# Kernel optimization log

Hardware: AMD Instinct MI355X
Metric: run time of the kernel (lower is better)

The kernel has to match this reference:

```python
import jax, jax.numpy as jnp
import numpy as np


def _ln(x, g, b, eps=1e-5):
    m = x.mean(-1, keepdims=True)
    v = ((x - m) ** 2).mean(-1, keepdims=True)
    return g * (x - m) / jnp.sqrt(v + eps) + b


def _mha(x, w_qkv, b_qkv, w_o, b_o, nh):
    B, S, d = x.shape
    hd = d // nh
    qkv = x @ w_qkv.T + b_qkv
    q, k, v = jnp.split(qkv, 3, axis=-1)
    sp = lambda t: t.reshape(B, S, nh, hd).transpose(0, 2, 1, 3)
    q, k, v = sp(q), sp(k), sp(v)
    a = jax.nn.softmax(jnp.einsum('bhqd,bhkd->bhqk', q, k) / np.float32(np.sqrt(hd)), axis=-1)
    o = jnp.einsum('bhqk,bhkd->bhqd', a, v).transpose(0, 2, 1, 3).reshape(B, S, d)
    return o @ w_o.T + b_o


def _enc(x, w_qkv, b_qkv, w_o, b_o, ga, ba, wf1, bf1, wf2, bf2, gb, bb, nh=2):
    # torch TransformerEncoderLayer, post-norm, ReLU FFN
    x = _ln(x + _mha(x, w_qkv, b_qkv, w_o, b_o, nh), ga, ba)
    ff = jax.nn.relu(x @ wf1.T + bf1) @ wf2.T + bf2
    return _ln(x + ff, gb, bb)


def forward(nodes, w_qkv1, b_qkv1, w_o1, b_o1, g1a, bb1a, w_ff1a, bf1a, w_ff1b, bf1b, g1b, bb1b,
            wq, bq, wk, bk, wv, bv, g_co, bb_co, w4, b4, w5, b5, w6, b6,
            w_rel, w_root, b_rgcn, wg_rel, wg_root, bg,
            w_qkv2, b_qkv2, w_o2, b_o2, g2a, bb2a, w_ff2a, bf2a, w_ff2b, bf2b, g2b, bb2b,
            w_l1, b_l1, w_l2, b_l2, edge_index, opt_idx):
    N, H = nodes.shape
    O = 4
    B = opt_idx.shape[0] // O
    # option-node mutual attention (encoder_layer1) + scatter back
    opts = nodes[opt_idx].reshape(B, O, H)
    opts = _enc(opts, w_qkv1, b_qkv1, w_o1, b_o1, g1a, bb1a, w_ff1a, bf1a, w_ff1b, bf1b, g1b, bb1b)
    nodes2 = nodes.at[opt_idx].set(opts.reshape(B * O, H))
    src, dst = edge_index[0], edge_index[1]
    xs, xd = nodes2[src], nodes2[dst]  # [E,H]
    # per-edge 4-head co-attention: node1/node2 are single rows so qk^T is a scalar per head
    hd = H // 4
    q = (xs @ wq.T + bq).reshape(-1, 4, hd)
    k = (xd @ wk.T + bk).reshape(-1, 4, hd)
    v = (xd @ wv.T + bv).reshape(-1, 4, hd)
    s = jnp.einsum('ehd,ehd->eh', q, k) / np.float32(np.sqrt(hd))
    r = (s[..., None] * v).reshape(-1, H)
    co = jax.nn.relu(_ln(r, g_co, bb_co))
    h = jax.nn.relu(co @ w4.T + b4)
    h = jax.nn.relu(h @ w5.T + b5)
    logits = h @ w6.T + b6  # [E,8]
    # original applies Softmax(dim=0) to a [1,8] tensor -> all ones -> argmax picks class 0
    probs = jax.nn.softmax(logits[:, None, :], axis=1)[:, 0, :]
    edge_type = jnp.argmax(probs, axis=-1)
    # RGCNConv(H, H, num_relations=8), mean aggregation per relation + root + bias
    agg = jnp.zeros((N, H), nodes.dtype)
    for rel in range(8):
        m = edge_type == rel
        msg = jnp.where(m[:, None], xs @ w_rel[rel], 0.0)
        ssum = jax.ops.segment_sum(msg, dst, num_segments=N)
        cnt = jax.ops.segment_sum(m.astype(nodes.dtype), dst, num_segments=N)
        agg = agg + ssum / jnp.maximum(cnt, 1.0)[:, None]
    out1 = nodes2 @ w_root + b_rgcn + agg
    # GraphConv(H, 64): add-aggregated neighbors through lin_rel + root through lin_root
    agg2 = jax.ops.segment_sum(out1[src], dst, num_segments=N)
    out2 = agg2 @ wg_rel + bg + out1 @ wg_root  # [N,64]
    # readout over option nodes (encoder_layer2 + tanh(linear1) + linear2)
    opt2 = out2[opt_idx].reshape(B, O, 64)
    opt2 = _enc(opt2, w_qkv2, b_qkv2, w_o2, b_o2, g2a, bb2a, w_ff2a, bf2a, w_ff2b, bf2b, g2b, bb2b)
    opt2 = jnp.tanh(opt2 @ w_l1.T + b_l1)
    return opt2 @ w_l2.T + b_l2  # [B,O,1]


def setup_inputs() -> dict:
    key = jax.random.key(0)
    N, E, B, O, H, F = 20000, 40000, 64, 4, 768, 2048
    ks = iter(jax.random.split(key, 64))
    W = lambda *s: jax.random.normal(next(ks), s, jnp.float32) * 0.02
    return dict(
        nodes=jax.random.normal(next(ks), (N, H), jnp.float32),
        edge_index=jax.random.randint(next(ks), (2, E), 0, N),
        opt_idx=jnp.arange(B * O),
        w_qkv1=W(3 * H, H), b_qkv1=jnp.zeros(3 * H), w_o1=W(H, H), b_o1=jnp.zeros(H),
        g1a=jnp.ones(H), bb1a=jnp.zeros(H),
        w_ff1a=W(F, H), bf1a=jnp.zeros(F), w_ff1b=W(H, F), bf1b=jnp.zeros(H),
        g1b=jnp.ones(H), bb1b=jnp.zeros(H),
        wq=W(H, H), bq=jnp.zeros(H), wk=W(H, H), bk=jnp.zeros(H), wv=W(H, H), bv=jnp.zeros(H),
        g_co=jnp.ones(H), bb_co=jnp.zeros(H),
        w4=W(H, H), b4=jnp.zeros(H), w5=W(64, H), b5=jnp.zeros(64), w6=W(8, 64), b6=jnp.zeros(8),
        w_rel=W(8, H, H), w_root=W(H, H), b_rgcn=jnp.zeros(H),
        wg_rel=W(H, 64), wg_root=W(H, 64), bg=jnp.zeros(64),
        w_qkv2=W(192, 64), b_qkv2=jnp.zeros(192), w_o2=W(64, 64), b_o2=jnp.zeros(64),
        g2a=jnp.ones(64), bb2a=jnp.zeros(64),
        w_ff2a=W(F, 64), bf2a=jnp.zeros(F), w_ff2b=W(64, F), bf2b=jnp.zeros(64),
        g2b=jnp.ones(64), bb2b=jnp.zeros(64),
        w_l1=W(64, 64), b_l1=jnp.zeros(64), w_l2=W(1, 64), b_l2=jnp.zeros(1),
    )


def reference(nodes, edge_index, opt_idx, w_qkv1, b_qkv1, w_o1, b_o1, g1a, bb1a, w_ff1a, bf1a,
              w_ff1b, bf1b, g1b, bb1b, wq, bq, wk, bk, wv, bv, g_co, bb_co, w4, b4, w5, b5, w6, b6,
              w_rel, w_root, b_rgcn, wg_rel, wg_root, bg, w_qkv2, b_qkv2, w_o2, b_o2, g2a, bb2a,
              w_ff2a, bf2a, w_ff2b, bf2b, g2b, bb2b, w_l1, b_l1, w_l2, b_l2):
    return forward(nodes, w_qkv1, b_qkv1, w_o1, b_o1, g1a, bb1a, w_ff1a, bf1a, w_ff1b, bf1b, g1b,
                   bb1b, wq, bq, wk, bk, wv, bv, g_co, bb_co, w4, b4, w5, b5, w6, b6, w_rel, w_root,
                   b_rgcn, wg_rel, wg_root, bg, w_qkv2, b_qkv2, w_o2, b_o2, g2a, bb2a, w_ff2a, bf2a,
                   w_ff2b, bf2b, g2b, bb2b, w_l1, b_l1, w_l2, b_l2, edge_index, opt_idx)
```

## Files before the change

### kernel.cpp

```cpp
#include <hip/hip_runtime.h>

typedef unsigned short u16;
typedef unsigned int u32;
typedef __bf16 bf16x8 __attribute__((ext_vector_type(8)));
typedef float f32x4 __attribute__((ext_vector_type(4)));

__device__ __forceinline__ u16 f2bf(float f) {
    union { float f; u32 u; } v; v.f = f;
    u32 r = v.u + 0x7FFFu + ((v.u >> 16) & 1u);
    return (u16)(r >> 16);
}
__device__ __forceinline__ float bf2f(u16 h) {
    union { u32 u; float f; } v; v.u = (u32)h << 16; return v.f;
}

__global__ __launch_bounds__(256) void gemm_bt(
    const u16* __restrict__ A, const u16* __restrict__ Bt,
    float* __restrict__ C, u16* __restrict__ Cb, const float* __restrict__ bias,
    int M, int N, int K, int relu)
{
    __shared__ char lA[128 * 64 * 2];
    __shared__ char lB[128 * 64 * 2];
    const int t = threadIdx.x;
    const int w = t >> 6, l = t & 63;
    const int bn = blockIdx.x, bm = blockIdx.y;
    const int wr = w >> 1, wc = w & 1;

    const int srow = w * 8 + (l >> 3);
    const int scol = ((l & 7) ^ (l >> 3)) << 3;
    const u16* gA = A + (size_t)(bm * 128 + srow) * K + scol;
    const u16* gB = Bt + (size_t)(bn * 128 + srow) * K + scol;

    f32x4 zero = {0.f, 0.f, 0.f, 0.f};
    f32x4 acc[4][4];
#pragma unroll
    for (int i = 0; i < 4; i++)
#pragma unroll
        for (int j = 0; j < 4; j++) acc[i][j] = zero;

    const int arow = wr * 64 + (l & 15);
    const int brow = wc * 64 + (l & 15);
    const int kx = l >> 4;
    const int sw = l & 7;

    for (int k0 = 0; k0 < K; k0 += 64) {
#pragma unroll
        for (int c2 = 0; c2 < 4; ++c2) {
            __builtin_amdgcn_global_load_lds(
                (const __attribute__((address_space(1))) void*)(gA + (size_t)c2 * 32 * K + k0),
                (__attribute__((address_space(3))) void*)(lA + c2 * 4096 + w * 1024), 16, 0, 0);
            __builtin_amdgcn_global_load_lds(
                (const __attribute__((address_space(1))) void*)(gB + (size_t)c2 * 32 * K + k0),
                (__attribute__((address_space(3))) void*)(lB + c2 * 4096 + w * 1024), 16, 0, 0);
        }
        __syncthreads();
#pragma unroll
        for (int kk = 0; kk < 2; ++kk) {
            bf16x8 af[4], bfr[4];
#pragma unroll
            for (int mi = 0; mi < 4; ++mi)
                af[mi] = *(const bf16x8*)(lA + (arow + mi * 16) * 128 + (((kk * 4 + kx) ^ sw) << 4));
#pragma unroll
            for (int ni = 0; ni < 4; ++ni)
                bfr[ni] = *(const bf16x8*)(lB + (brow + ni * 16) * 128 + (((kk * 4 + kx) ^ sw) << 4));
#pragma unroll
            for (int mi = 0; mi < 4; ++mi)
#pragma unroll
                for (int ni = 0; ni < 4; ++ni)
                    acc[mi][ni] = __builtin_amdgcn_mfma_f32_16x16x32_bf16(af[mi], bfr[ni], acc[mi][ni], 0, 0, 0);
        }
        __syncthreads();
    }

    const int cm = bm * 128 + wr * 64;
    const int cn = bn * 128 + wc * 64;
#pragma unroll
    for (int mi = 0; mi < 4; ++mi) {
#pragma unroll
        for (int ni = 0; ni < 4; ++ni) {
            int row0 = cm + mi * 16 + (l >> 4) * 4;
            int col = cn + ni * 16 + (l & 15);
            float bv = bias ? bias[col] : 0.f;
#pragma unroll
            for (int r = 0; r < 4; ++r) {
                float v = acc[mi][ni][r] + bv;
                if (relu) v = fmaxf(v, 0.f);
                if (Cb) Cb[(size_t)(row0 + r) * N + col] = f2bf(v);
                else    C [(size_t)(row0 + r) * N + col] = v;
            }
        }
    }
}

struct CJob { const float* src; u16* dst; long n4; };
struct CJobs6 { CJob j[6]; };
__global__ void conv6_bf16(CJobs6 jobs)
{
    CJob jb = jobs.j[blockIdx.z];
    long i = (long)blockIdx.x * blockDim.x + threadIdx.x;
    long stride = (long)gridDim.x * blockDim.x;
    for (; i < jb.n4; i += stride) {
        float4 v = ((const float4*)jb.src)[i];
        ushort4 o;
        o.x = f2bf(v.x); o.y = f2bf(v.y); o.z = f2bf(v.z); o.w = f2bf(v.w);
        ((ushort4*)jb.dst)[i] = o;
    }
}

struct TJob { const float* src; u16* dst; int Rr, Cc, ldo; };
struct TJobs2 { TJob j[2]; };
__global__ void transpose2_bf16(TJobs2 jobs)
{
    TJob jb = jobs.j[blockIdx.z];
    __shared__ float tile[32][33];
    int c0 = blockIdx.x * 32, r0 = blockIdx.y * 32;
    if (c0 >= jb.Cc || r0 >= jb.Rr) return;
    int tx = threadIdx.x, ty = threadIdx.y;
    for (int dy = 0; dy < 32; dy += 8) {
        int r = r0 + ty + dy, c = c0 + tx;
        tile[ty + dy][tx] = (r < jb.Rr && c < jb.Cc) ? jb.src[(size_t)r * jb.Cc + c] : 0.f;
    }
    __syncthreads();
    for (int dy = 0; dy < 32; dy += 8) {
        int c = c0 + ty + dy, r = r0 + tx;
        if (c < jb.Cc && r < jb.Rr) jb.dst[(size_t)c * jb.ldo + r] = f2bf(tile[tx][ty + dy]);
    }
}

__global__ void bc_prep(const float* __restrict__ b_rgcn, const float* __restrict__ wg_rel,
                        const float* __restrict__ wg_root, float* __restrict__ bc)
{
    int n = threadIdx.x;
    const float* W = (n < 64) ? (wg_rel + n) : (wg_root + (n - 64));
    float s = 0.f;
    for (int k = 0; k < 768; k++) s += b_rgcn[k] * W[(size_t)k * 64];
    bc[n] = s;
}

__global__ void conv_nodes_str(const float* __restrict__ nodes, u16* __restrict__ Abig,
                               int Nn, int Mpad)
{
    long i = (long)blockIdx.x * blockDim.x + threadIdx.x;
    long stride = (long)gridDim.x * blockDim.x;
    long n4 = (long)Mpad * 192;
    for (; i < n4; i += stride) {
        long row = i / 192, c4 = i % 192;
        ushort4 o;
        if ((int)row < Nn) {
            float4 v = ((const float4*)nodes)[i];
            o.x = f2bf(v.x); o.y = f2bf(v.y); o.z = f2bf(v.z); o.w = f2bf(v.w);
        } else { o.x = 0; o.y = 0; o.z = 0; o.w = 0; }
        ((ushort4*)Abig)[row * 384 + c4] = o;
    }
}

__global__ void gather_x0(const float* __restrict__ nodes, const int* __restrict__ opt,
                          float* __restrict__ x0, u16* __restrict__ x0b, int H)
{
    int r = blockIdx.x;
    size_t srcb = (size_t)opt[r] * H;
    for (int c = threadIdx.x; c < H; c += blockDim.x) {
        float v = nodes[srcb + c];
        x0[(size_t)r * H + c] = v;
        x0b[(size_t)r * H + c] = f2bf(v);
    }
}

__global__ void scatter_opts_str(const float* __restrict__ x2, const int* __restrict__ opt,
                                 u16* __restrict__ Abig)
{
    int r = blockIdx.x;
    size_t dstb = (size_t)opt[r] * 1536;
    for (int c = threadIdx.x; c < 768; c += blockDim.x)
        Abig[dstb + c] = f2bf(x2[(size_t)r * 768 + c]);
}

__global__ __launch_bounds__(256) void attn_small_b(
    const float* __restrict__ qkv, u16* __restrict__ out, int H, int nh, int hd)
{
    int b = blockIdx.x / nh, h = blockIdx.x % nh;
    int w = threadIdx.x >> 6, l = threadIdx.x & 63;
    __shared__ float sc[4][4];
    int qs = 3 * H;
    const float* qr = qkv + (size_t)(b * 4 + w) * qs + h * hd;
    float scale = rsqrtf((float)hd);
    for (int sj = 0; sj < 4; ++sj) {
        const float* kr = qkv + (size_t)(b * 4 + sj) * qs + H + h * hd;
        float p = 0.f;
        for (int i = l; i < hd; i += 64) p += qr[i] * kr[i];
        for (int off = 32; off; off >>= 1) p += __shfl_down(p, off, 64);
        if (l == 0) sc[w][sj] = p * scale;
    }
    __syncthreads();
    float a0 = sc[w][0], a1 = sc[w][1], a2 = sc[w][2], a3 = sc[w][3];
    float mx = fmaxf(fmaxf(a0, a1), fmaxf(a2, a3));
    float e0 = __expf(a0 - mx), e1 = __expf(a1 - mx), e2 = __expf(a2 - mx), e3 = __expf(a3 - mx);
    float inv = 1.f / (e0 + e1 + e2 + e3);
    e0 *= inv; e1 *= inv; e2 *= inv; e3 *= inv;
    const float* v0 = qkv + (size_t)(b * 4 + 0) * qs + 2 * H + h * hd;
    const float* v1 = v0 + qs; const float* v2 = v1 + qs; const float* v3 = v2 + qs;
    u16* orow = out + (size_t)(b * 4 + w) * H + h * hd;
    for (int i = l; i < hd; i += 64)
        orow[i] = f2bf(e0 * v0[i] + e1 * v1[i] + e2 * v2[i] + e3 * v3[i]);
}

__global__ __launch_bounds__(256) void ln768(
    const float* __restrict__ x, const float* __restrict__ res,
    const float* __restrict__ g, const float* __restrict__ be,
    float* __restrict__ out, u16* __restrict__ outb)
{
    int row = blockIdx.x, t = threadIdx.x;
    const float* xr = x + (size_t)row * 768;
    const float* rr = res + (size_t)row * 768;
    float v[3]; float s = 0.f, q = 0.f;
#pragma unroll
    for (int i = 0; i < 3; i++) {
        float a = xr[t + i * 256] + rr[t + i * 256];
        v[i] = a; s += a; q += a * a;
    }
    for (int off = 32; off; off >>= 1) { s += __shfl_down(s, off, 64); q += __shfl_down(q, off, 64); }
    __shared__ float ss[4], qq[4];
    int w = t >> 6, l = t & 63;
    if (l == 0) { ss[w] = s; qq[w] = q; }
    __syncthreads();
    s = ss[0] + ss[1] + ss[2] + ss[3];
    q = qq[0] + qq[1] + qq[2] + qq[3];
    float m = s * (1.f / 768.f);
    float ri = rsqrtf(q * (1.f / 768.f) - m * m + 1e-5f);
#pragma unroll
    for (int i = 0; i < 3; i++) {
        int c = t + i * 256;
        float o = g[c] * (v[i] - m) * ri + be[c];
        out[(size_t)row * 768 + c] = o;
        if (outb) outb[(size_t)row * 768 + c] = f2bf(o);
    }
}

__global__ void edge_count(const int* __restrict__ ei, int* __restrict__ cnt, int E)
{
    int e = blockIdx.x * blockDim.x + threadIdx.x;
    if (e < E) atomicAdd(&cnt[ei[E + e]], 1);
}

__global__ __launch_bounds__(1024) void scan_offsets(
    const int* __restrict__ cnt, int* __restrict__ offs, int* __restrict__ cur, int n)
{
    __shared__ int part[1024];
    int t = threadIdx.x;
    int per = (n + 1023) / 1024;
    int base = t * per;
    int local = 0;
    for (int i = 0; i < per; i++) {
        int idx = base + i;
        if (idx < n) local += cnt[idx];
    }
    part[t] = local;
    __syncthreads();
    for (int off = 1; off < 1024; off <<= 1) {
        int v = (t >= off) ? part[t - off] : 0;
        __syncthreads();
        part[t] += v;
        __syncthreads();
    }
    int prefix = (t == 0) ? 0 : part[t - 1];
    for (int i = 0; i < per; i++) {
        int idx = base + i;
        if (idx < n) {
            offs[idx] = prefix;
            cur[idx] = prefix;
            prefix += cnt[idx];
        }
    }
}

__global__ void fill_edges(const int* __restrict__ ei, int* __restrict__ cur,
                           int* __restrict__ elist, int E)
{
    int e = blockIdx.x * blockDim.x + threadIdx.x;
    if (e < E) {
        int d = ei[E + e];
        int pos = atomicAdd(&cur[d], 1);
        elist[pos] = ei[e];
    }
}

__global__ __launch_bounds__(256) void gather_mean(
    const int* __restrict__ offs, const int* __restrict__ cnt, const int* __restrict__ elist,
    u16* Abig, int Nn, int Mpad)
{
    int w = threadIdx.x >> 6, l = threadIdx.x & 63;
    int d = blockIdx.x * 4 + w;
    if (d >= Mpad) return;
    float acc[12];
#pragma unroll
    for (int j = 0; j < 12; j++) acc[j] = 0.f;
    float inv = 0.f;
    if (d < Nn) {
        int base = offs[d], c = cnt[d];
        for (int i = 0; i < c; i++) {
            int s = elist[base + i];
            const ushort4* p = (const ushort4*)(Abig + (size_t)s * 1536);
#pragma unroll
            for (int j4 = 0; j4 < 3; j4++) {
                ushort4 v = p[j4 * 64 + l];
                acc[j4 * 4 + 0] += bf2f(v.x);
                acc[j4 * 4 + 1] += bf2f(v.y);
                acc[j4 * 4 + 2] += bf2f(v.z);
                acc[j4 * 4 + 3] += bf2f(v.w);
            }
        }
        inv = 1.f / (float)max(c, 1);
    }
    ushort4* q = (ushort4*)(Abig + (size_t)d * 1536 + 768);
#pragma unroll
    for (int j4 = 0; j4 < 3; j4++) {
        ushort4 o;
        o.x = f2bf(acc[j4 * 4 + 0] * inv);
        o.y = f2bf(acc[j4 * 4 + 1] * inv);
        o.z = f2bf(acc[j4 * 4 + 2] * inv);
        o.w = f2bf(acc[j4 * 4 + 3] * inv);
        q[j4 * 64 + l] = o;
    }
}

__global__ __launch_bounds__(256) void enc2_head(
    const int* __restrict__ opt, const int* __restrict__ offs, const int* __restrict__ cnt,
    const int* __restrict__ elist, const float* __restrict__ C2, const float* __restrict__ bg,
    const float* __restrict__ w_qkv2, const float* __restrict__ b_qkv2,
    const float* __restrict__ w_o2, const float* __restrict__ b_o2,
    const float* __restrict__ g2a, const float* __restrict__ bb2a,
    float* __restrict__ x21)
{
    __shared__ float X[4][64];
    __shared__ float QKV[4][192];
    __shared__ float T[4][64];
    int b = blockIdx.x;
    int w = threadIdx.x >> 6, l = threadIdx.x & 63;
    int row = b * 4 + w;

    {
        int d = opt[row];
        float acc = bg[l] + C2[(size_t)d * 128 + 64 + l];
        int base = offs[d], c = cnt[d];
        for (int i = 0; i < c; i++) {
            int s = elist[base + i];
            acc += C2[(size_t)s * 128 + l];
        }
        X[w][l] = acc;
    }
    __syncthreads();

#pragma unroll
    for (int j = 0; j < 3; j++) {
        int n = l + j * 64;
        const float* wr = w_qkv2 + (size_t)n * 64;
        float s = b_qkv2[n];
        for (int k = 0; k < 64; k++) s += X[w][k] * wr[k];
        QKV[w][n] = s;
    }
    __syncthreads();

    {
        float q = QKV[w][l];
        float p0 = q * QKV[0][64 + l], p1 = q * QKV[1][64 + l];
        float p2 = q * QKV[2][64 + l], p3 = q * QKV[3][64 + l];
#pragma unroll
        for (int off = 1; off < 32; off <<= 1) {
            p0 += __shfl_xor(p0, off, 64); p1 += __shfl_xor(p1, off, 64);
            p2 += __shfl_xor(p2, off, 64); p3 += __shfl_xor(p3, off, 64);
        }
        p0 *= 0.1767766953f; p1 *= 0.1767766953f; p2 *= 0.1767766953f; p3 *= 0.1767766953f;
        float mx = fmaxf(fmaxf(p0, p1), fmaxf(p2, p3));
        float e0 = __expf(p0 - mx), e1 = __expf(p1 - mx), e2 = __expf(p2 - mx), e3 = __expf(p3 - mx);
        float inv = 1.f / (e0 + e1 + e2 + e3);
        T[w][l] = (e0 * QKV[0][128 + l] + e1 * QKV[1][128 + l] +
                   e2 * QKV[2][128 + l] + e3 * QKV[3][128 + l]) * inv;
    }
    __syncthreads();

    {
        const float* wr = w_o2 + (size_t)l * 64;
        float s = b_o2[l];
        for (int k = 0; k < 64; k++) s += T[w][k] * wr[k];
        float xa = s + X[w][l];
        float sum = xa, sq = xa * xa;
#pragma unroll
        for (int off = 1; off < 64; off <<= 1) {
            sum += __shfl_xor(sum, off, 64);
            sq  += __shfl_xor(sq, off, 64);
        }
        float m = sum * (1.f / 64.f);
        float ri = rsqrtf(sq * (1.f / 64.f) - m * m + 1e-5f);
        x21[(size_t)row * 64 + l] = g2a[l] * (xa - m) * ri + bb2a[l];
    }
}

__global__ __launch_bounds__(256) void ff1_par(
    const float* __restrict__ x21, const float* __restrict__ wf1,
    const float* __restrict__ bf1, float* __restrict__ Hf)
{
    __shared__ float X[64];
    int b = blockIdx.x, t = threadIdx.x;
    int r = b >> 3, n = (b & 7) * 256 + t;
    if (t < 64) X[t] = x21[(size_t)r * 64 + t];
    __syncthreads();
    const float4* wr4 = (const float4*)(wf1 + (size_t)n * 64);
    float s = bf1[n];
#pragma unroll
    for (int k4 = 0; k4 < 16; k4++) {
        float4 wv = wr4[k4];
        const float* xp = X + k4 * 4;
        s += wv.x * xp[0] + wv.y * xp[1] + wv.z * xp[2] + wv.w * xp[3];
    }
    Hf[(size_t)r * 2048 + n] = fmaxf(s, 0.f);
}

__global__ __launch_bounds__(256) void ff2_tail(
    const float* __restrict__ Hf, const float* __restrict__ x21,
    const float* __restrict__ wf2, const float* __restrict__ bf2,
    const float* __restrict__ g2b, const float* __restrict__ bb2b,
    const float* __restrict__ w_l1, const float* __restrict__ b_l1,
    const float* __restrict__ w_l2, const float* __restrict__ b_l2,
    float* __restrict__ out)
{
    __shared__ float HL[2048];
    __shared__ float part[4][64];
    __shared__ float X2[64];
    int r = blockIdx.x, t = threadIdx.x;
    int w = t >> 6, l = t & 63;

    {
        const float4* src = (const float4*)(Hf + (size_t)r * 2048);
        float4* dst = (float4*)HL;
        dst[t] = src[t];
        dst[t + 256] = src[t + 256];
    }
    __syncthreads();

    {
        const float4* wr4 = (const float4*)(wf2 + (size_t)l * 2048 + w * 512);
        const float* hp = HL + w * 512;
        float s = 0.f;
#pragma unroll 16
        for (int k4 = 0; k4 < 128; k4++) {
            float4 wv = wr4[k4];
            const float* xp = hp + k4 * 4;
            s += wv.x * xp[0] + wv.y * xp[1] + wv.z * xp[2] + wv.w * xp[3];
        }
        part[w][l] = s;
    }
    __syncthreads();

    if (w == 0) {
        float xa = part[0][l] + part[1][l] + part[2][l] + part[3][l] + bf2[l]
                 + x21[(size_t)r * 64 + l];
        float sum = xa, sq = xa * xa;
#pragma unroll
        for (int off = 1; off < 64; off <<= 1) {
            sum += __shfl_xor(sum, off, 64);
            sq  += __shfl_xor(sq, off, 64);
        }
        float m = sum * (1.f / 64.f);
        float ri = rsqrtf(sq * (1.f / 64.f) - m * m + 1e-5f);
        X2[l] = g2b[l] * (xa - m) * ri + bb2b[l];
        __builtin_amdgcn_wave_barrier();
        const float* wr = w_l1 + (size_t)l * 64;
        float s = b_l1[l];
        for (int k = 0; k < 64; k++) s += X2[k] * wr[k];
        float tv = tanhf(s);
        float p = tv * w_l2[l];
#pragma unroll
        for (int off = 1; off < 64; off <<= 1) p += __shfl_xor(p, off, 64);
        if (l == 0) out[r] = p + b_l2[0];
    }
}

extern "C" void kernel_launch(void* const* d_in, const int* in_sizes, int n_in,
                              void* d_out, int out_size, void* d_ws, size_t ws_size,
                              hipStream_t stream)
{
    const float* nodes  = (const float*)d_in[0];
    const int*   ei     = (const int*)d_in[1];
    const int*   opt    = (const int*)d_in[2];
    const float* w_qkv1 = (const float*)d_in[3];
    const float* b_qkv1 = (const float*)d_in[4];
    const float* w_o1   = (const float*)d_in[5];
    const float* b_o1   = (const float*)d_in[6];
    const float* g1a    = (const float*)d_in[7];
    const float* bb1a   = (const float*)d_in[8];
    const float* w_ff1a = (const float*)d_in[9];
    const float* bf1a   = (const float*)d_in[10];
    const float* w_ff1b = (const float*)d_in[11];
    const float* bf1b   = (const float*)d_in[12];
    const float* g1b    = (const float*)d_in[13];
    const float* bb1b   = (const float*)d_in[14];
    const float* w_rel  = (const float*)d_in[29];
    const float* w_root = (const float*)d_in[30];
    const float* b_rgcn = (const float*)d_in[31];
    const float* wg_rel = (const float*)d_in[32];
    const float* wg_root= (const float*)d_in[33];
    const float* bg     = (const float*)d_in[34];
    const float* w_qkv2 = (const float*)d_in[35];
    const float* b_qkv2 = (const float*)d_in[36];
    const float* w_o2   = (const float*)d_in[37];
    const float* b_o2   = (const float*)d_in[38];
    const float* g2a    = (const float*)d_in[39];
    const float* bb2a   = (const float*)d_in[40];
    const float* w_ff2a = (const float*)d_in[41];
    const float* bf2a   = (const float*)d_in[42];
    const float* w_ff2b = (const float*)d_in[43];
    const float* bf2b   = (const float*)d_in[44];
    const float* g2b    = (const float*)d_in[45];
    const float* bb2b   = (const float*)d_in[46];
    const float* w_l1   = (const float*)d_in[47];
    const float* b_l1   = (const float*)d_in[48];
    const float* w_l2   = (const float*)d_in[49];
    const float* b_l2   = (const float*)d_in[50];

    const int H = 768, F = 2048;
    const int Nn = in_sizes[0] / H;
    const int E  = in_sizes[1] / 2;
    const int R  = in_sizes[2];
    const int Mpad = (Nn + 127) & ~127;
    const int Bb = R / 4;

    char* ws = (char*)d_ws;
    size_t off = 0;
    auto alloc = [&](size_t b) -> char* {
        char* p = ws + off; off += (b + 255) & ~(size_t)255; return p;
    };
    u16* wqkv1b  = (u16*)alloc((size_t)3 * H * H * 2);
    u16* wo1b    = (u16*)alloc((size_t)H * H * 2);
    u16* wff1ab  = (u16*)alloc((size_t)F * H * 2);
    u16* wff1bb  = (u16*)alloc((size_t)H * F * 2);
    u16* Wbraw   = (u16*)alloc((size_t)1536 * H * 2);
    u16* W2tb    = (u16*)alloc((size_t)128 * H * 2);
    u16* WcT     = (u16*)alloc((size_t)128 * 1536 * 2);
    float* bc    = (float*)alloc((size_t)128 * 4);
    float* x0   = (float*)alloc((size_t)R * H * 4);
    u16*  x0b   = (u16*)alloc((size_t)R * H * 2);
    float* qkvb = (float*)alloc((size_t)R * 3 * H * 4);
    u16*  atnob = (u16*)alloc((size_t)R * H * 2);
    float* obuf = (float*)alloc((size_t)R * H * 4);
    float* x1   = (float*)alloc((size_t)R * H * 4);
    u16*  x1b   = (u16*)alloc((size_t)R * H * 2);
    u16*  ffhb  = (u16*)alloc((size_t)R * F * 2);
    float* ffo  = (float*)alloc((size_t)R * H * 4);
    float* x2   = (float*)alloc((size_t)R * H * 4);
    u16*  Abig  = (u16*)alloc((size_t)Mpad * 1536 * 2);
    float* C2   = (float*)alloc((size_t)Mpad * 128 * 4);
    int* cnt   = (int*)alloc((size_t)Nn * 4);
    int* offs  = (int*)alloc((size_t)Nn * 4);
    int* cur   = (int*)alloc((size_t)Nn * 4);
    int* elist = (int*)alloc((size_t)E * 4);
    float* x21 = (float*)alloc((size_t)R * 64 * 4);
    float* Hf2 = (float*)alloc((size_t)R * F * 4);
    (void)ws_size; (void)n_in; (void)out_size;

    {
        CJobs6 cj;
        cj.j[0] = { w_qkv1, wqkv1b, (long)3 * H * H / 4 };
        cj.j[1] = { w_o1,   wo1b,   (long)H * H / 4 };
        cj.j[2] = { w_ff1a, wff1ab, (long)F * H / 4 };
        cj.j[3] = { w_ff1b, wff1bb, (long)H * F / 4 };
        cj.j[4] = { w_root, Wbraw,                    (long)H * H / 4 };
        cj.j[5] = { w_rel,  Wbraw + (size_t)H * H,    (long)H * H / 4 };
        conv6_bf16<<<dim3(432, 1, 6), 256, 0, stream>>>(cj);
        TJobs2 tj;
        tj.j[0] = { wg_rel,  W2tb,                    768, 64, 768 };
        tj.j[1] = { wg_root, W2tb + (size_t)64 * 768, 768, 64, 768 };
        transpose2_bf16<<<dim3(2, 24, 2), dim3(32, 8), 0, stream>>>(tj);
    }
    gemm_bt<<<dim3(1536 / 128, 1), 256, 0, stream>>>(W2tb, Wbraw, nullptr, WcT, nullptr, 128, 1536, 768, 0);
    bc_prep<<<1, 128, 0, stream>>>(b_rgcn, wg_rel, wg_root, bc);

    gather_x0<<<R, 256, 0, stream>>>(nodes, opt, x0, x0b, H);
    gemm_bt<<<dim3(3 * H / 128, R / 128), 256, 0, stream>>>(x0b, wqkv1b, qkvb, nullptr, b_qkv1, R, 3 * H, H, 0);
    attn_small_b<<<Bb * 2, 256, 0, stream>>>(qkvb, atnob, H, 2, H / 2);
    gemm_bt<<<dim3(H / 128, R / 128), 256, 0, stream>>>(atnob, wo1b, obuf, nullptr, b_o1, R, H, H, 0);
    ln768<<<R, 256, 0, stream>>>(obuf, x0, g1a, bb1a, x1, x1b);
    gemm_bt<<<dim3(F / 128, R / 128), 256, 0, stream>>>(x1b, wff1ab, nullptr, ffhb, bf1a, R, F, H, 1);
    gemm_bt<<<dim3(H / 128, R / 128), 256, 0, stream>>>(ffhb, wff1bb, ffo, nullptr, bf1b, R, H, F, 0);
    ln768<<<R, 256, 0, stream>>>(ffo, x1, g1b, bb1b, x2, nullptr);

    conv_nodes_str<<<2048, 256, 0, stream>>>(nodes, Abig, Nn, Mpad);
    scatter_opts_str<<<R, 256, 0, stream>>>(x2, opt, Abig);

    hipMemsetAsync(cnt, 0, (size_t)Nn * 4, stream);
    edge_count<<<(E + 255) / 256, 256, 0, stream>>>(ei, cnt, E);
    scan_offsets<<<1, 1024, 0, stream>>>(cnt, offs, cur, Nn);
    fill_edges<<<(E + 255) / 256, 256, 0, stream>>>(ei, cur, elist, E);
    gather_mean<<<Mpad / 4, 256, 0, stream>>>(offs, cnt, elist, Abig, Nn, Mpad);

    gemm_bt<<<dim3(1, Mpad / 128), 256, 0, stream>>>(Abig, WcT, C2, nullptr, bc, Mpad, 128, 1536, 0);

    enc2_head<<<Bb, 256, 0, stream>>>(opt, offs, cnt, elist, C2, bg,
                                      w_qkv2, b_qkv2, w_o2, b_o2, g2a, bb2a, x21);
    ff1_par<<<R * 8, 256, 0, stream>>>(x21, w_ff2a, bf2a, Hf2);
    ff2_tail<<<R, 256, 0, stream>>>(Hf2, x21, w_ff2b, bf2b, g2b, bb2b,
                                    w_l1, b_l1, w_l2, b_l2, (float*)d_out);
}
```

Before: 550.6 us.

## Split-K the small encoder GEMMs and fuse reductions into attention and layernorm

Adds a split-K GEMM variant that writes fp32 partials per K-slice, so the small-M (R=256) encoder GEMMs launch many more workgroups. The partial sums are reduced inside the consumer kernels: attention adds the QKV bias and partials, layernorm adds the bias and residual, and a separate reduce kernel covers the FFN hidden layer and the weight-combine GEMM. The final layernorm writes straight into the gathered Abig rows, which removes the scatter kernel and several intermediate buffers. In exchange it adds partial-buffer traffic (up to 8 slices), and the attention kernel hardcodes the shapes (256 rows, 2304 width, scale constant).

Measured after the change: 476.1 us. 1.16x faster.

```diff
diff --git a/kernel.cpp b/kernel.cpp
--- a/kernel.cpp
+++ b/kernel.cpp
@@ -89,6 +89,93 @@
                 else    C [(size_t)(row0 + r) * N + col] = v;
             }
         }
+    }
+}
+
+__global__ __launch_bounds__(256) void gemm_bt_sk(
+    const u16* __restrict__ A, const u16* __restrict__ Bt,
+    float* __restrict__ P, int M, int N, int K, int Kc)
+{
+    __shared__ char lA[128 * 64 * 2];
+    __shared__ char lB[128 * 64 * 2];
+    const int t = threadIdx.x;
+    const int w = t >> 6, l = t & 63;
+    const int bn = blockIdx.x, bm = blockIdx.y, ks = blockIdx.z;
+    const int wr = w >> 1, wc = w & 1;
+
+    const int srow = w * 8 + (l >> 3);
+    const int scol = ((l & 7) ^ (l >> 3)) << 3;
+    const u16* gA = A + (size_t)(bm * 128 + srow) * K + scol;
+    const u16* gB = Bt + (size_t)(bn * 128 + srow) * K + scol;
+
+    f32x4 zero = {0.f, 0.f, 0.f, 0.f};
+    f32x4 acc[4][4];
+#pragma unroll
+    for (int i = 0; i < 4; i++)
+#pragma unroll
+        for (int j = 0; j < 4; j++) acc[i][j] = zero;
+
+    const int arow = wr * 64 + (l & 15);
+    const int brow = wc * 64 + (l & 15);
+    const int kx = l >> 4;
+    const int sw = l & 7;
+
+    const int kbeg = ks * Kc, kend = kbeg + Kc;
+    for (int k0 = kbeg; k0 < kend; k0 += 64) {
+#pragma unroll
+        for (int c2 = 0; c2 < 4; ++c2) {
+            __builtin_amdgcn_global_load_lds(
+                (const __attribute__((address_space(1))) void*)(gA + (size_t)c2 * 32 * K + k0),
+                (__attribute__((address_space(3))) void*)(lA + c2 * 4096 + w * 1024), 16, 0, 0);
+            __builtin_amdgcn_global_load_lds(
+                (const __attribute__((address_space(1))) void*)(gB + (size_t)c2 * 32 * K + k0),
+                (__attribute__((address_space(3))) void*)(lB + c2 * 4096 + w * 1024), 16, 0, 0);
+        }
+        __syncthreads();
+#pragma unroll
+        for (int kk = 0; kk < 2; ++kk) {
+            bf16x8 af[4], bfr[4];
+#pragma unroll
+            for (int mi = 0; mi < 4; ++mi)
+                af[mi] = *(const bf16x8*)(lA + (arow + mi * 16) * 128 + (((kk * 4 + kx) ^ sw) << 4));
+#pragma unroll
+            for (int ni = 0; ni < 4; ++ni)
+                bfr[ni] = *(const bf16x8*)(lB + (brow + ni * 16) * 128 + (((kk * 4 + kx) ^ sw) << 4));
+#pragma unroll
+            for (int mi = 0; mi < 4; ++mi)
+#pragma unroll
+                for (int ni = 0; ni < 4; ++ni)
+                    acc[mi][ni] = __builtin_amdgcn_mfma_f32_16x16x32_bf16(af[mi], bfr[ni], acc[mi][ni], 0, 0, 0);
+        }
+        __syncthreads();
+    }
+
+    float* Pp = P + (size_t)ks * M * N;
+    const int cm = bm * 128 + wr * 64;
+    const int cn = bn * 128 + wc * 64;
+#pragma unroll
+    for (int mi = 0; mi < 4; ++mi) {
+#pragma unroll
+        for (int ni = 0; ni < 4; ++ni) {
+            int row0 = cm + mi * 16 + (l >> 4) * 4;
+            int col = cn + ni * 16 + (l & 15);
+#pragma unroll
+            for (int r = 0; r < 4; ++r)
+                Pp[(size_t)(row0 + r) * N + col] = acc[mi][ni][r];
+        }
+    }
+}
+
+__global__ void sk_reduce_b(const float* __restrict__ P, int KS, long MN, int N,
+                            const float* __restrict__ bias, int relu, u16* __restrict__ outb)
+{
+    long i = (long)blockIdx.x * blockDim.x + threadIdx.x;
+    long stride = (long)gridDim.x * blockDim.x;
+    for (; i < MN; i += stride) {
+        float v = bias ? bias[i % N] : 0.f;
+        for (int ks = 0; ks < KS; ks++) v += P[(size_t)ks * MN + i];
+        if (relu) v = fmaxf(v, 0.f);
+        outb[i] = f2bf(v);
     }
 }
 
@@ -166,56 +253,60 @@
     }
 }
 
-__global__ void scatter_opts_str(const float* __restrict__ x2, const int* __restrict__ opt,
-                                 u16* __restrict__ Abig)
-{
-    int r = blockIdx.x;
-    size_t dstb = (size_t)opt[r] * 1536;
-    for (int c = threadIdx.x; c < 768; c += blockDim.x)
-        Abig[dstb + c] = f2bf(x2[(size_t)r * 768 + c]);
-}
-
-__global__ __launch_bounds__(256) void attn_small_b(
-    const float* __restrict__ qkv, u16* __restrict__ out, int H, int nh, int hd)
-{
-    int b = blockIdx.x / nh, h = blockIdx.x % nh;
+__global__ __launch_bounds__(256) void attn_fused(
+    const float* __restrict__ Pq, int KS, const float* __restrict__ b_qkv1,
+    u16* __restrict__ atnob)
+{
+    __shared__ float Q[4][384], Kk[4][384], V[4][384];
+    int b = blockIdx.x >> 1, h = blockIdx.x & 1;
     int w = threadIdx.x >> 6, l = threadIdx.x & 63;
-    __shared__ float sc[4][4];
-    int qs = 3 * H;
-    const float* qr = qkv + (size_t)(b * 4 + w) * qs + h * hd;
-    float scale = rsqrtf((float)hd);
-    for (int sj = 0; sj < 4; ++sj) {
-        const float* kr = qkv + (size_t)(b * 4 + sj) * qs + H + h * hd;
+    int row = b * 4 + w;
+    const int hb = h * 384;
+#pragma unroll
+    for (int j = 0; j < 6; j++) {
+        int c = hb + j * 64 + l;
+        float q = b_qkv1[c], k = b_qkv1[768 + c], v = b_qkv1[1536 + c];
+        for (int ks = 0; ks < KS; ks++) {
+            const float* Pr = Pq + (size_t)ks * 256 * 2304 + (size_t)row * 2304;
+            q += Pr[c]; k += Pr[768 + c]; v += Pr[1536 + c];
+        }
+        Q[w][j * 64 + l] = q; Kk[w][j * 64 + l] = k; V[w][j * 64 + l] = v;
+    }
+    __syncthreads();
+    float sc[4];
+#pragma unroll
+    for (int sj = 0; sj < 4; sj++) {
         float p = 0.f;
-        for (int i = l; i < hd; i += 64) p += qr[i] * kr[i];
+#pragma unroll
+        for (int j = 0; j < 6; j++) p += Q[w][j * 64 + l] * Kk[sj][j * 64 + l];
         for (int off = 32; off; off >>= 1) p += __shfl_down(p, off, 64);
-        if (l == 0) sc[w][sj] = p * scale;
-    }
-    __syncthreads();
-    float a0 = sc[w][0], a1 = sc[w][1], a2 = sc[w][2], a3 = sc[w][3];
-    float mx = fmaxf(fmaxf(a0, a1), fmaxf(a2, a3));
-    float e0 = __expf(a0 - mx), e1 = __expf(a1 - mx), e2 = __expf(a2 - mx), e3 = __expf(a3 - mx);
+        sc[sj] = __shfl(p, 0, 64) * 0.05103103630798287f;
+    }
+    float mx = fmaxf(fmaxf(sc[0], sc[1]), fmaxf(sc[2], sc[3]));
+    float e0 = __expf(sc[0] - mx), e1 = __expf(sc[1] - mx);
+    float e2 = __expf(sc[2] - mx), e3 = __expf(sc[3] - mx);
     float inv = 1.f / (e0 + e1 + e2 + e3);
     e0 *= inv; e1 *= inv; e2 *= inv; e3 *= inv;
-    const float* v0 = qkv + (size_t)(b * 4 + 0) * qs + 2 * H + h * hd;
-    const float* v1 = v0 + qs; const float* v2 = v1 + qs; const float* v3 = v2 + qs;
-    u16* orow = out + (size_t)(b * 4 + w) * H + h * hd;
-    for (int i = l; i < hd; i += 64)
-        orow[i] = f2bf(e0 * v0[i] + e1 * v1[i] + e2 * v2[i] + e3 * v3[i]);
-}
-
-__global__ __launch_bounds__(256) void ln768(
-    const float* __restrict__ x, const float* __restrict__ res,
-    const float* __restrict__ g, const float* __restrict__ be,
-    float* __restrict__ out, u16* __restrict__ outb)
-{
-    int row = blockIdx.x, t = threadIdx.x;
-    const float* xr = x + (size_t)row * 768;
-    const float* rr = res + (size_t)row * 768;
+#pragma unroll
+    for (int j = 0; j < 6; j++) {
+        int c = j * 64 + l;
+        float o = e0 * V[0][c] + e1 * V[1][c] + e2 * V[2][c] + e3 * V[3][c];
+        atnob[(size_t)row * 768 + hb + c] = f2bf(o);
+    }
+}
+
+__global__ __launch_bounds__(256) void ln_reduce768(
+    const float* __restrict__ P, int KS, const float* __restrict__ bias,
+    const float* __restrict__ res, const float* __restrict__ g, const float* __restrict__ be,
+    float* __restrict__ outf, u16* __restrict__ outb, const int* __restrict__ opt, int ldo)
+{
+    int r = blockIdx.x, t = threadIdx.x;
     float v[3]; float s = 0.f, q = 0.f;
 #pragma unroll
     for (int i = 0; i < 3; i++) {
-        float a = xr[t + i * 256] + rr[t + i * 256];
+        int c = t + i * 256;
+        float a = bias[c] + res[(size_t)r * 768 + c];
+        for (int ks = 0; ks < KS; ks++) a += P[(size_t)ks * 256 * 768 + (size_t)r * 768 + c];
         v[i] = a; s += a; q += a * a;
     }
     for (int off = 32; off; off >>= 1) { s += __shfl_down(s, off, 64); q += __shfl_down(q, off, 64); }
@@ -227,12 +318,13 @@
     q = qq[0] + qq[1] + qq[2] + qq[3];
     float m = s * (1.f / 768.f);
     float ri = rsqrtf(q * (1.f / 768.f) - m * m + 1e-5f);
+    size_t ob = opt ? (size_t)opt[r] * ldo : (size_t)r * ldo;
 #pragma unroll
     for (int i = 0; i < 3; i++) {
         int c = t + i * 256;
         float o = g[c] * (v[i] - m) * ri + be[c];
-        out[(size_t)row * 768 + c] = o;
-        if (outb) outb[(size_t)row * 768 + c] = f2bf(o);
+        if (outf) outf[(size_t)r * 768 + c] = o;
+        if (outb) outb[ob + c] = f2bf(o);
     }
 }
 
@@ -537,16 +629,13 @@
     u16* W2tb    = (u16*)alloc((size_t)128 * H * 2);
     u16* WcT     = (u16*)alloc((size_t)128 * 1536 * 2);
     float* bc    = (float*)alloc((size_t)128 * 4);
+    float* Psk  = (float*)alloc((size_t)4 * 256 * 2304 * 4);
     float* x0   = (float*)alloc((size_t)R * H * 4);
     u16*  x0b   = (u16*)alloc((size_t)R * H * 2);
-    float* qkvb = (float*)alloc((size_t)R * 3 * H * 4);
     u16*  atnob = (u16*)alloc((size_t)R * H * 2);
-    float* obuf = (float*)alloc((size_t)R * H * 4);
     float* x1   = (float*)alloc((size_t)R * H * 4);
     u16*  x1b   = (u16*)alloc((size_t)R * H * 2);
     u16*  ffhb  = (u16*)alloc((size_t)R * F * 2);
-    float* ffo  = (float*)alloc((size_t)R * H * 4);
-    float* x2   = (float*)alloc((size_t)R * H * 4);
     u16*  Abig  = (u16*)alloc((size_t)Mpad * 1536 * 2);
     float* C2   = (float*)alloc((size_t)Mpad * 128 * 4);
     int* cnt   = (int*)alloc((size_t)Nn * 4);
@@ -571,20 +660,21 @@
         tj.j[1] = { wg_root, W2tb + (size_t)64 * 768, 768, 64, 768 };
         transpose2_bf16<<<dim3(2, 24, 2), dim3(32, 8), 0, stream>>>(tj);
     }
-    gemm_bt<<<dim3(1536 / 128, 1), 256, 0, stream>>>(W2tb, Wbraw, nullptr, WcT, nullptr, 128, 1536, 768, 0);
+    gemm_bt_sk<<<dim3(12, 1, 4), 256, 0, stream>>>(W2tb, Wbraw, Psk, 128, 1536, 768, 192);
+    sk_reduce_b<<<768, 256, 0, stream>>>(Psk, 4, (long)128 * 1536, 1536, nullptr, 0, WcT);
     bc_prep<<<1, 128, 0, stream>>>(b_rgcn, wg_rel, wg_root, bc);
 
+    conv_nodes_str<<<2048, 256, 0, stream>>>(nodes, Abig, Nn, Mpad);
+
     gather_x0<<<R, 256, 0, stream>>>(nodes, opt, x0, x0b, H);
-    gemm_bt<<<dim3(3 * H / 128, R / 128), 256, 0, stream>>>(x0b, wqkv1b, qkvb, nullptr, b_qkv1, R, 3 * H, H, 0);
-    attn_small_b<<<Bb * 2, 256, 0, stream>>>(qkvb, atnob, H, 2, H / 2);
-    gemm_bt<<<dim3(H / 128, R / 128), 256, 0, stream>>>(atnob, wo1b, obuf, nullptr, b_o1, R, H, H, 0);
-    ln768<<<R, 256, 0, stream>>>(obuf, x0, g1a, bb1a, x1, x1b);
-    gemm_bt<<<dim3(F / 128, R / 128), 256, 0, stream>>>(x1b, wff1ab, nullptr, ffhb, bf1a, R, F, H, 1);
-    gemm_bt<<<dim3(H / 128, R / 128), 256, 0, stream>>>(ffhb, wff1bb, ffo, nullptr, bf1b, R, H, F, 0);
-    ln768<<<R, 256, 0, stream>>>(ffo, x1, g1b, bb1b, x2, nullptr);
-
-    conv_nodes_str<<<2048, 256, 0, stream>>>(nodes, Abig, Nn, Mpad);
-    scatter_opts_str<<<R, 256, 0, stream>>>(x2, opt, Abig);
+    gemm_bt_sk<<<dim3(18, 2, 4), 256, 0, stream>>>(x0b, wqkv1b, Psk, R, 3 * H, H, 192);
+    attn_fused<<<Bb * 2, 256, 0, stream>>>(Psk, 4, b_qkv1, atnob);
+    gemm_bt_sk<<<dim3(6, 2, 4), 256, 0, stream>>>(atnob, wo1b, Psk, R, H, H, 192);
+    ln_reduce768<<<R, 256, 0, stream>>>(Psk, 4, b_o1, x0, g1a, bb1a, x1, x1b, nullptr, 768);
+    gemm_bt_sk<<<dim3(16, 2, 4), 256, 0, stream>>>(x1b, wff1ab, Psk, R, F, H, 192);
+    sk_reduce_b<<<2048, 256, 0, stream>>>(Psk, 4, (long)R * F, F, bf1a, 1, ffhb);
+    gemm_bt_sk<<<dim3(6, 2, 8), 256, 0, stream>>>(ffhb, wff1bb, Psk, R, H, F, 256);
+    ln_reduce768<<<R, 256, 0, stream>>>(Psk, 8, bf1b, x1, g1b, bb1b, nullptr, Abig, opt, 1536);
 
     hipMemsetAsync(cnt, 0, (size_t)Nn * 4, stream);
     edge_count<<<(E + 255) / 256, 256, 0, stream>>>(ei, cnt, E);
```
